# Performance work log

Hardware: AMD Instinct MI355X
Metric: run time of the kernel (lower is better)

Reference implementation:

```python
import jax, jax.numpy as jnp
import numpy as np

B, T, C, H = 2, 2048, 1024, 16
HD = C // H  # 64
EPS = 1e-5


def _ln(x, g, b):
    mu = jnp.mean(x, axis=-1, keepdims=True)
    var = jnp.var(x, axis=-1, keepdims=True)
    return (x - mu) * jax.lax.rsqrt(var + EPS) * g + b


def setup_inputs() -> dict:
    key = jax.random.key(0)
    ks = jax.random.split(key, 8)
    s = lambda n: 1.0 / np.sqrt(n)
    return {
        "x": jax.random.normal(ks[0], (B, T, C), dtype=jnp.float32),
        "ln1_g": jnp.ones((C,), jnp.float32), "ln1_b": jnp.zeros((C,), jnp.float32),
        "ln2_g": jnp.ones((C,), jnp.float32), "ln2_b": jnp.zeros((C,), jnp.float32),
        "w_in": jax.random.normal(ks[1], (C, 3 * C), jnp.float32) * s(C),
        "b_in": jnp.zeros((3 * C,), jnp.float32),
        "w_out": jax.random.normal(ks[2], (C, C), jnp.float32) * s(C),
        "b_out": jnp.zeros((C,), jnp.float32),
        "w_fc": jax.random.normal(ks[3], (C, 4 * C), jnp.float32) * s(C),
        "b_fc": jnp.zeros((4 * C,), jnp.float32),
        "w_proj": jax.random.normal(ks[4], (4 * C, C), jnp.float32) * s(4 * C),
        "b_proj": jnp.zeros((C,), jnp.float32),
    }


def reference(x, ln1_g, ln1_b, ln2_g, ln2_b, w_in, b_in, w_out, b_out,
              w_fc, b_fc, w_proj, b_proj):
    # --- residual 1: x + attn(ln1(x)) ---
    h = _ln(x, ln1_g, ln1_b)
    qkv = h @ w_in + b_in                          # (B,T,3C)
    # reshape to (B,T,H,3*HD) then chunk per head (matches torch code exactly)
    qkv = qkv.reshape(B, T, H, 3 * HD).transpose(0, 2, 1, 3)  # (B,H,T,3*HD)
    q, k, v = jnp.split(qkv, 3, axis=-1)           # each (B,H,T,HD)
    att = jnp.einsum('bhqd,bhkd->bhqk', q, k) / np.sqrt(HD)
    causal = jnp.tril(jnp.ones((T, T), bool))
    att = jnp.where(causal, att, -jnp.inf)
    att = jax.nn.softmax(att, axis=-1)
    o = jnp.einsum('bhqk,bhkd->bhqd', att, v)      # (B,H,T,HD)
    o = o.transpose(0, 2, 1, 3).reshape(B, T, C)
    x1 = x + (o @ w_out + b_out)
    # --- ln2 applied to residual stream, then residual 2 on top of ln2 output ---
    y = _ln(x1, ln2_g, ln2_b)
    mlp = jax.nn.gelu(y @ w_fc + b_fc, approximate=False) @ w_proj + b_proj
    return y + mlp
```

## Files before the change

### kernel.cpp

```cpp
#include <hip/hip_runtime.h>
#include <hip/hip_bf16.h>
#include <math.h>

typedef __bf16 bf16;
typedef __bf16 bf16x8 __attribute__((ext_vector_type(8)));
typedef __bf16 bf16x4 __attribute__((ext_vector_type(4)));
typedef float floatx4 __attribute__((ext_vector_type(4)));

#define B_ 2
#define T_ 2048
#define C_ 1024
#define H_ 16
#define HD_ 64

__device__ __forceinline__ void gload_lds16(const bf16* g, bf16* l) {
    __builtin_amdgcn_global_load_lds(
        (const __attribute__((address_space(1))) unsigned int*)(g),
        (__attribute__((address_space(3))) unsigned int*)(l), 16, 0, 0);
}

__global__ void transpose_all(const float* __restrict__ w_in, const float* __restrict__ w_out,
                              const float* __restrict__ w_fc, const float* __restrict__ w_proj,
                              bf16* __restrict__ o_in, bf16* __restrict__ o_out,
                              bf16* __restrict__ o_fc, bf16* __restrict__ o_proj) {
    int t = blockIdx.x;
    const float* src; bf16* dst; int K, N, idx;
    if (t < 3072)      { src = w_in;   dst = o_in;   K = 1024; N = 3072; idx = t; }
    else if (t < 4096) { src = w_out;  dst = o_out;  K = 1024; N = 1024; idx = t - 3072; }
    else if (t < 8192) { src = w_fc;   dst = o_fc;   K = 1024; N = 4096; idx = t - 4096; }
    else               { src = w_proj; dst = o_proj; K = 4096; N = 1024; idx = t - 8192; }
    int ntx = N >> 5;
    int nt = (idx % ntx) * 32, kt = (idx / ntx) * 32;
    __shared__ float tile[32][33];
    int tx = threadIdx.x, ty = threadIdx.y;
    #pragma unroll
    for (int i = 0; i < 32; i += 8)
        tile[ty + i][tx] = src[(size_t)(kt + ty + i) * N + nt + tx];
    __syncthreads();
    #pragma unroll
    for (int i = 0; i < 32; i += 8)
        dst[(size_t)(nt + ty + i) * K + kt + tx] = (bf16)tile[tx][ty + i];
}

__global__ __launch_bounds__(256) void ln_kernel(const float* __restrict__ x,
                                                 const float* __restrict__ g,
                                                 const float* __restrict__ b,
                                                 bf16* __restrict__ out_b,
                                                 float* __restrict__ out_f) {
    int row = blockIdx.x;
    int tid = threadIdx.x;
    const float* xr = x + (size_t)row * C_;
    float4 v = ((const float4*)xr)[tid];
    float s  = v.x + v.y + v.z + v.w;
    float ss = v.x * v.x + v.y * v.y + v.z * v.z + v.w * v.w;
    #pragma unroll
    for (int off = 32; off; off >>= 1) {
        s  += __shfl_down(s, off);
        ss += __shfl_down(ss, off);
    }
    __shared__ float red[8];
    int wid = tid >> 6;
    if ((tid & 63) == 0) { red[wid] = s; red[wid + 4] = ss; }
    __syncthreads();
    s  = red[0] + red[1] + red[2] + red[3];
    ss = red[4] + red[5] + red[6] + red[7];
    float mean = s * (1.0f / C_);
    float var  = ss * (1.0f / C_) - mean * mean;
    float rstd = rsqrtf(var + 1e-5f);
    float4 gv = ((const float4*)g)[tid];
    float4 bv = ((const float4*)b)[tid];
    float o0 = (v.x - mean) * rstd * gv.x + bv.x;
    float o1 = (v.y - mean) * rstd * gv.y + bv.y;
    float o2 = (v.z - mean) * rstd * gv.z + bv.z;
    float o3 = (v.w - mean) * rstd * gv.w + bv.w;
    bf16x4 ob = { (bf16)o0, (bf16)o1, (bf16)o2, (bf16)o3 };
    ((bf16x4*)out_b)[(size_t)row * 256 + tid] = ob;
    if (out_f) {
        float4 of; of.x = o0; of.y = o1; of.z = o2; of.w = o3;
        ((float4*)out_f)[(size_t)row * 256 + tid] = of;
    }
}

__device__ __forceinline__ float gelu_exact(float v) {
    return 0.5f * v * (1.0f + erff(v * 0.70710678118654752f));
}

template<int TN, int MODE>
__global__ __launch_bounds__(256) void gemm128(const bf16* __restrict__ A,
                                               const bf16* __restrict__ Bt,
                                               const float* __restrict__ bias,
                                               const float* __restrict__ add,
                                               void* __restrict__ out,
                                               int M, int N, int K) {
    constexpr int BN = TN / 32;
    __shared__ __align__(16) bf16 As[128 * 64];
    __shared__ __align__(16) bf16 Bs[TN * 64];

    int m0 = blockIdx.y * 128, n0 = blockIdx.x * TN;
    int tid = threadIdx.x;
    int wid = __builtin_amdgcn_readfirstlane(tid >> 6);
    int lane = tid & 63;
    int lm = lane & 15, quad = lane >> 4;
    int wm = (wid & 1) * 64;
    int wn = (wid >> 1) * (TN / 2);
    int lrow = lane >> 3;
    int lcol = (lane & 7) * 8;

    const bf16* Ablk = A  + (size_t)m0 * K;
    const bf16* Bblk = Bt + (size_t)n0 * K;

    floatx4 acc[4][BN];
    #pragma unroll
    for (int i = 0; i < 4; i++)
        #pragma unroll
        for (int j = 0; j < BN; j++) { floatx4 z = {0.f, 0.f, 0.f, 0.f}; acc[i][j] = z; }

    for (int k0 = 0; k0 < K; k0 += 64) {
        __syncthreads();
        #pragma unroll
        for (int c = 0; c < 4; c++) {
            int row = wid * 32 + c * 8;
            gload_lds16(Ablk + (size_t)(row + lrow) * K + k0 + lcol, As + row * 64);
        }
        #pragma unroll
        for (int c = 0; c < TN / 32; c++) {
            int row = wid * (TN / 4) + c * 8;
            gload_lds16(Bblk + (size_t)(row + lrow) * K + k0 + lcol, Bs + row * 64);
        }
        __syncthreads();
        #pragma unroll
        for (int kc = 0; kc < 2; kc++) {
            bf16x8 af[4], bfr[BN];
            #pragma unroll
            for (int i = 0; i < 4; i++)
                af[i] = *(const bf16x8*)(As + (wm + i * 16 + lm) * 64 + kc * 32 + quad * 8);
            #pragma unroll
            for (int j = 0; j < BN; j++)
                bfr[j] = *(const bf16x8*)(Bs + (wn + j * 16 + lm) * 64 + kc * 32 + quad * 8);
            #pragma unroll
            for (int i = 0; i < 4; i++)
                #pragma unroll
                for (int j = 0; j < BN; j++)
                    acc[i][j] = __builtin_amdgcn_mfma_f32_16x16x32_bf16(af[i], bfr[j], acc[i][j], 0, 0, 0);
        }
    }

    #pragma unroll
    for (int i = 0; i < 4; i++)
        #pragma unroll
        for (int j = 0; j < BN; j++) {
            int mbase = m0 + wm + i * 16 + quad * 4;
            int n     = n0 + wn + j * 16 + lm;
            float bsn = bias[n];
            #pragma unroll
            for (int r = 0; r < 4; r++) {
                size_t idx = (size_t)(mbase + r) * N + n;
                float v = acc[i][j][r] + bsn;
                if (MODE == 1) v = gelu_exact(v);
                if (MODE == 2) { ((float*)out)[idx] = v + add[idx]; }
                else           { ((bf16*)out)[idx] = (bf16)v; }
            }
        }
}

template<int MODE>
__global__ __launch_bounds__(256) void gemm_nrw(const bf16* __restrict__ A,
                                                const bf16* __restrict__ Bt,
                                                const float* __restrict__ bias,
                                                const float* __restrict__ add,
                                                void* __restrict__ out,
                                                int M, int N, int K) {
    __shared__ __align__(16) bf16 As[2][128 * 64];
    __shared__ __align__(16) bf16 Bs[2][64 * 64];

    int lin = blockIdx.x;
    int xcd = lin & 7, loc = lin >> 3;
    int m0 = (((xcd << 2) | (loc & 3))) * 128;
    int n0 = (loc >> 2) * 64;
    int tid = threadIdx.x;
    int wid = __builtin_amdgcn_readfirstlane(tid >> 6);
    int lane = tid & 63;
    int lm = lane & 15, quad = lane >> 4;
    int wm = (wid & 1) * 64;
    int wn = (wid >> 1) * 32;
    int lrow = lane >> 3;
    int lcol = (lane & 7) * 8;

    const bf16* Ablk = A  + (size_t)m0 * K;
    const bf16* Bblk = Bt + (size_t)n0 * K;

    floatx4 acc[4][2];
    #pragma unroll
    for (int i = 0; i < 4; i++)
        #pragma unroll
        for (int j = 0; j < 2; j++) { floatx4 z = {0.f, 0.f, 0.f, 0.f}; acc[i][j] = z; }

    #pragma unroll
    for (int c = 0; c < 4; c++) {
        int row = wid * 32 + c * 8;
        gload_lds16(Ablk + (size_t)(row + lrow) * K + lcol, &As[0][row * 64]);
    }
    #pragma unroll
    for (int c = 0; c < 2; c++) {
        int row = wid * 16 + c * 8;
        gload_lds16(Bblk + (size_t)(row + lrow) * K + lcol, &Bs[0][row * 64]);
    }

    int cur = 0;
    for (int k0 = 0; k0 < K; k0 += 64, cur ^= 1) {
        int nxt = cur ^ 1;
        if (k0 + 64 < K) {
            __builtin_amdgcn_s_barrier();
            __asm__ volatile("" ::: "memory");
            #pragma unroll
            for (int c = 0; c < 4; c++) {
                int row = wid * 32 + c * 8;
                gload_lds16(Ablk + (size_t)(row + lrow) * K + (k0 + 64) + lcol, &As[nxt][row * 64]);
            }
            #pragma unroll
            for (int c = 0; c < 2; c++) {
                int row = wid * 16 + c * 8;
                gload_lds16(Bblk + (size_t)(row + lrow) * K + (k0 + 64) + lcol, &Bs[nxt][row * 64]);
            }
            __asm__ volatile("s_waitcnt vmcnt(6)" ::: "memory");
        } else {
            __asm__ volatile("s_waitcnt vmcnt(0)" ::: "memory");
        }
        __builtin_amdgcn_s_barrier();
        __asm__ volatile("" ::: "memory");
        #pragma unroll
        for (int kc = 0; kc < 2; kc++) {
            bf16x8 af[4], bfr[2];
            #pragma unroll
            for (int i = 0; i < 4; i++)
                af[i] = *(const bf16x8*)(&As[cur][(wm + i * 16 + lm) * 64 + kc * 32 + quad * 8]);
            #pragma unroll
            for (int j = 0; j < 2; j++)
                bfr[j] = *(const bf16x8*)(&Bs[cur][(wn + j * 16 + lm) * 64 + kc * 32 + quad * 8]);
            #pragma unroll
            for (int i = 0; i < 4; i++)
                #pragma unroll
                for (int j = 0; j < 2; j++)
                    acc[i][j] = __builtin_amdgcn_mfma_f32_16x16x32_bf16(af[i], bfr[j], acc[i][j], 0, 0, 0);
        }
    }

    #pragma unroll
    for (int i = 0; i < 4; i++)
        #pragma unroll
        for (int j = 0; j < 2; j++) {
            int mbase = m0 + wm + i * 16 + quad * 4;
            int n     = n0 + wn + j * 16 + lm;
            float bsn = bias[n];
            #pragma unroll
            for (int r = 0; r < 4; r++) {
                size_t idx = (size_t)(mbase + r) * N + n;
                float v = acc[i][j][r] + bsn;
                if (MODE == 1) v = gelu_exact(v);
                if (MODE == 2) { ((float*)out)[idx] = v + add[idx]; }
                else           { ((bf16*)out)[idx] = (bf16)v; }
            }
        }
}

#define QT_ 128
#define KT_ 64

__global__ __launch_bounds__(256) void attn_mfma_kernel(const bf16* __restrict__ qkv,
                                                        bf16* __restrict__ o) {
    int bh = blockIdx.x;
    int b = bh >> 4, h = bh & 15;
    int q0 = (gridDim.y - 1 - blockIdx.y) * QT_;
    int tid = threadIdx.x, wid = tid >> 6, lane = tid & 63;
    int wm = wid * 32;
    int lm = lane & 15, quad = lane >> 4;
    int sw = lm & 7;

    const bf16* base = qkv + (size_t)b * T_ * (3 * C_) + h * (3 * HD_);

    __shared__ __align__(16) bf16 Ks[KT_][72];
    __shared__ __align__(16) bf16 Vt[HD_][72];
    __shared__ __align__(16) bf16 PsT[4][32][64];

    bf16x8 qf[2][2];
    #pragma unroll
    for (int am = 0; am < 2; am++)
        #pragma unroll
        for (int kc = 0; kc < 2; kc++) {
            int r = q0 + wm + am * 16 + lm;
            qf[am][kc] = *(const bf16x8*)(base + (size_t)r * (3 * C_) + kc * 32 + quad * 8);
        }

    floatx4 acc_o[2][4];
    #pragma unroll
    for (int am = 0; am < 2; am++)
        #pragma unroll
        for (int dn = 0; dn < 4; dn++) { floatx4 z = {0.f, 0.f, 0.f, 0.f}; acc_o[am][dn] = z; }
    float mst[2] = { -1e30f, -1e30f };
    float lst[2] = { 0.0f, 0.0f };

    int scol = (tid & 7) * 8;

    int kmax = q0 + QT_;
    for (int k0 = 0; k0 < kmax; k0 += KT_) {
        int kr0 = tid >> 3;
        bf16x8 kv0 = *(const bf16x8*)(base + (size_t)(k0 + kr0)      * (3 * C_) + HD_ + scol);
        bf16x8 kv1 = *(const bf16x8*)(base + (size_t)(k0 + kr0 + 32) * (3 * C_) + HD_ + scol);
        bf16x8 vv0 = *(const bf16x8*)(base + (size_t)(k0 + kr0)      * (3 * C_) + 2 * HD_ + scol);
        bf16x8 vv1 = *(const bf16x8*)(base + (size_t)(k0 + kr0 + 32) * (3 * C_) + 2 * HD_ + scol);
        __syncthreads();
        *(bf16x8*)(&Ks[kr0][scol])      = kv0;
        *(bf16x8*)(&Ks[kr0 + 32][scol]) = kv1;
        {
            int c = scol >> 3;
            int pk0 = (((kr0)       >> 3) ^ c) * 8 + (kr0 & 7);
            int pk1 = (((kr0 + 32)  >> 3) ^ c) * 8 + (kr0 & 7);
            #pragma unroll
            for (int j = 0; j < 8; j++) {
                Vt[scol + j][pk0] = vv0[j];
                Vt[scol + j][pk1] = vv1[j];
            }
        }
        __syncthreads();

        if (k0 <= q0 + wm + 31) {
            floatx4 st[4][2];
            #pragma unroll
            for (int bn = 0; bn < 4; bn++)
                #pragma unroll
                for (int am = 0; am < 2; am++) { floatx4 z = {0.f, 0.f, 0.f, 0.f}; st[bn][am] = z; }
            #pragma unroll
            for (int kc = 0; kc < 2; kc++) {
                bf16x8 kf[4];
                #pragma unroll
                for (int bn = 0; bn < 4; bn++)
                    kf[bn] = *(const bf16x8*)(&Ks[bn * 16 + lm][kc * 32 + quad * 8]);
                #pragma unroll
                for (int bn = 0; bn < 4; bn++)
                    #pragma unroll
                    for (int am = 0; am < 2; am++)
                        st[bn][am] = __builtin_amdgcn_mfma_f32_16x16x32_bf16(kf[bn], qf[am][kc], st[bn][am], 0, 0, 0);
            }

            float alpha_s[2];
            #pragma unroll
            for (int am = 0; am < 2; am++) {
                int gq = q0 + wm + am * 16 + lm;
                int need_mask = (k0 + KT_ - 1) > (q0 + wm + am * 16);
                float vv[4][4];
                float rm = -1e30f;
                #pragma unroll
                for (int bn = 0; bn < 4; bn++)
                    #pragma unroll
                    for (int r = 0; r < 4; r++) {
                        float sv = st[bn][am][r] * 0.125f;
                        int key = k0 + bn * 16 + quad * 4 + r;
                        sv = (!need_mask || key <= gq) ? sv : -1e30f;
                        vv[bn][r] = sv;
                        rm = fmaxf(rm, sv);
                    }
                rm = fmaxf(rm, __shfl_xor(rm, 16));
                rm = fmaxf(rm, __shfl_xor(rm, 32));
                float mold = mst[am];
                float mnew = fmaxf(mold, rm);
                float alpha = __expf(mold - mnew);
                mst[am] = mnew;
                float ps = 0.f;
                #pragma unroll
                for (int bn = 0; bn < 4; bn++) {
                    float p0 = __expf(vv[bn][0] - mnew);
                    float p1 = __expf(vv[bn][1] - mnew);
                    float p2 = __expf(vv[bn][2] - mnew);
                    float p3 = __expf(vv[bn][3] - mnew);
                    ps += (p0 + p1) + (p2 + p3);
                    bf16x4 pk = { (bf16)p0, (bf16)p1, (bf16)p2, (bf16)p3 };
                    int kb = bn * 2 + (quad >> 1);
                    int col = ((kb ^ sw) << 3) + (quad & 1) * 4;
                    *(bf16x4*)(&PsT[wid][am * 16 + lm][col]) = pk;
                }
                ps += __shfl_xor(ps, 16);
                ps += __shfl_xor(ps, 32);
                lst[am] = lst[am] * alpha + ps;
                alpha_s[am] = alpha;
            }

            #pragma unroll
            for (int am = 0; am < 2; am++)
                #pragma unroll
                for (int r = 0; r < 4; r++) {
                    float ar = __shfl(alpha_s[am], quad * 4 + r);
                    #pragma unroll
                    for (int dn = 0; dn < 4; dn++) acc_o[am][dn][r] *= ar;
                }

            __asm__ volatile("s_waitcnt lgkmcnt(0)" ::: "memory");

            #pragma unroll
            for (int kc = 0; kc < 2; kc++) {
                bf16x8 pa[2], vfr[4];
                #pragma unroll
                for (int am = 0; am < 2; am++)
                    pa[am] = *(const bf16x8*)(&PsT[wid][am * 16 + lm][((kc * 4 + quad) ^ sw) << 3]);
                #pragma unroll
                for (int dn = 0; dn < 4; dn++) {
                    int d = dn * 16 + lm;
                    int swd = (d >> 3) & 7;
                    vfr[dn] = *(const bf16x8*)(&Vt[d][(((kc * 4 + quad) ^ swd) << 3)]);
                }
                #pragma unroll
                for (int am = 0; am < 2; am++)
                    #pragma unroll
                    for (int dn = 0; dn < 4; dn++)
                        acc_o[am][dn] = __builtin_amdgcn_mfma_f32_16x16x32_bf16(pa[am], vfr[dn], acc_o[am][dn], 0, 0, 0);
            }
        }
    }

    #pragma unroll
    for (int am = 0; am < 2; am++) {
        float il = 1.0f / lst[am];
        #pragma unroll
        for (int r = 0; r < 4; r++) {
            float ir = __shfl(il, quad * 4 + r);
            int qrow = q0 + wm + am * 16 + quad * 4 + r;
            bf16* orow = o + ((size_t)b * T_ + qrow) * C_ + h * HD_;
            #pragma unroll
            for (int dn = 0; dn < 4; dn++)
                orow[dn * 16 + lm] = (bf16)(acc_o[am][dn][r] * ir);
        }
    }
}

extern "C" void kernel_launch(void* const* d_in, const int* in_sizes, int n_in,
                              void* d_out, int out_size, void* d_ws, size_t ws_size,
                              hipStream_t stream) {
    (void)in_sizes; (void)n_in; (void)out_size; (void)ws_size;
    const float* x      = (const float*)d_in[0];
    const float* ln1_g  = (const float*)d_in[1];
    const float* ln1_b  = (const float*)d_in[2];
    const float* ln2_g  = (const float*)d_in[3];
    const float* ln2_b  = (const float*)d_in[4];
    const float* w_in   = (const float*)d_in[5];
    const float* b_in   = (const float*)d_in[6];
    const float* w_out  = (const float*)d_in[7];
    const float* b_out  = (const float*)d_in[8];
    const float* w_fc   = (const float*)d_in[9];
    const float* b_fc   = (const float*)d_in[10];
    const float* w_proj = (const float*)d_in[11];
    const float* b_proj = (const float*)d_in[12];

    char* ws = (char*)d_ws;
    const size_t MB = 1024 * 1024;
    bf16*  w_inT   = (bf16*)(ws + 0);
    bf16*  w_outT  = (bf16*)(ws + 6 * MB);
    bf16*  w_fcT   = (bf16*)(ws + 8 * MB);
    bf16*  w_projT = (bf16*)(ws + 16 * MB);
    bf16*  qkv     = (bf16*)(ws + 24 * MB);
    bf16*  fc_act  = (bf16*)(ws + 24 * MB);
    bf16*  o_buf   = (bf16*)(ws + 56 * MB);
    bf16*  y_b     = (bf16*)(ws + 56 * MB);
    bf16*  h_b     = (bf16*)(ws + 64 * MB);
    float* x1      = (float*)(ws + 64 * MB);
    float* y_f     = (float*)(ws + 80 * MB);

    const int M = B_ * T_;

    transpose_all<<<12288, dim3(32, 8), 0, stream>>>(w_in, w_out, w_fc, w_proj,
                                                     w_inT, w_outT, w_fcT, w_projT);

    ln_kernel<<<M, 256, 0, stream>>>(x, ln1_g, ln1_b, h_b, nullptr);
    gemm128<128, 0><<<dim3(3 * C_ / 128, M / 128), 256, 0, stream>>>(h_b, w_inT, b_in, nullptr,
                                                                     qkv, M, 3 * C_, C_);
    attn_mfma_kernel<<<dim3(B_ * H_, T_ / QT_), 256, 0, stream>>>(qkv, o_buf);
    gemm_nrw<2><<<dim3((C_ / 64) * (M / 128)), 256, 0, stream>>>(o_buf, w_outT, b_out, x,
                                                                 x1, M, C_, C_);
    ln_kernel<<<M, 256, 0, stream>>>(x1, ln2_g, ln2_b, y_b, y_f);
    gemm128<128, 1><<<dim3(4 * C_ / 128, M / 128), 256, 0, stream>>>(y_b, w_fcT, b_fc, nullptr,
                                                                     fc_act, M, 4 * C_, C_);
    gemm_nrw<2><<<dim3((C_ / 64) * (M / 128)), 256, 0, stream>>>(fc_act, w_projT, b_proj, y_f,
                                                                 (float*)d_out, M, C_, 4 * C_);
}
```

Measured before the change: 391.1 us.

## Store activations and weights in MFMA fragment layout for LDS-free out/proj GEMMs

```diff
diff --git a/kernel.cpp b/kernel.cpp
--- a/kernel.cpp
+++ b/kernel.cpp
@@ -13,33 +13,57 @@
 #define H_ 16
 #define HD_ 64
 
+
 __device__ __forceinline__ void gload_lds16(const bf16* g, bf16* l) {
     __builtin_amdgcn_global_load_lds(
         (const __attribute__((address_space(1))) unsigned int*)(g),
         (__attribute__((address_space(3))) unsigned int*)(l), 16, 0, 0);
 }
 
-__global__ void transpose_all(const float* __restrict__ w_in, const float* __restrict__ w_out,
-                              const float* __restrict__ w_fc, const float* __restrict__ w_proj,
-                              bf16* __restrict__ o_in, bf16* __restrict__ o_out,
-                              bf16* __restrict__ o_fc, bf16* __restrict__ o_proj) {
+__global__ __launch_bounds__(256) void transpose_all(
+        const float* __restrict__ w_in, const float* __restrict__ w_out,
+        const float* __restrict__ w_fc, const float* __restrict__ w_proj,
+        bf16* __restrict__ o_in, bf16* __restrict__ o_out,
+        bf16* __restrict__ o_fc, bf16* __restrict__ o_proj) {
+    __shared__ float shf[64 * 33];
     int t = blockIdx.x;
-    const float* src; bf16* dst; int K, N, idx;
-    if (t < 3072)      { src = w_in;   dst = o_in;   K = 1024; N = 3072; idx = t; }
-    else if (t < 4096) { src = w_out;  dst = o_out;  K = 1024; N = 1024; idx = t - 3072; }
-    else if (t < 8192) { src = w_fc;   dst = o_fc;   K = 1024; N = 4096; idx = t - 4096; }
-    else               { src = w_proj; dst = o_proj; K = 4096; N = 1024; idx = t - 8192; }
-    int ntx = N >> 5;
-    int nt = (idx % ntx) * 32, kt = (idx / ntx) * 32;
-    __shared__ float tile[32][33];
-    int tx = threadIdx.x, ty = threadIdx.y;
-    #pragma unroll
-    for (int i = 0; i < 32; i += 8)
-        tile[ty + i][tx] = src[(size_t)(kt + ty + i) * N + nt + tx];
-    __syncthreads();
-    #pragma unroll
-    for (int i = 0; i < 32; i += 8)
-        dst[(size_t)(nt + ty + i) * K + kt + tx] = (bf16)tile[tx][ty + i];
+    int tid = threadIdx.x;
+    if (t < 7168) {
+        const float* src; bf16* dst; int K, N, idx;
+        if (t < 3072) { src = w_in; dst = o_in; K = 1024; N = 3072; idx = t; }
+        else          { src = w_fc; dst = o_fc; K = 1024; N = 4096; idx = t - 3072; }
+        int ntx = N >> 5;
+        int nt = (idx % ntx) * 32, kt = (idx / ntx) * 32;
+        int tx = tid & 31, ty = tid >> 5;
+        #pragma unroll
+        for (int i = 0; i < 32; i += 8)
+            shf[(ty + i) * 33 + tx] = src[(size_t)(kt + ty + i) * N + nt + tx];
+        __syncthreads();
+        #pragma unroll
+        for (int i = 0; i < 32; i += 8)
+            dst[(size_t)(nt + ty + i) * K + kt + tx] = (bf16)shf[tx * 33 + ty + i];
+    } else {
+        const float* src; bf16* dst; int K, idx;
+        if (t < 7680) { src = w_out;  dst = o_out;  K = 1024; idx = t - 7168; }
+        else          { src = w_proj; dst = o_proj; K = 4096; idx = t - 7680; }
+        const int N = 1024;
+        int n0 = (idx & 31) * 32, k0 = (idx >> 5) * 64;
+        int col = tid & 31, kr = tid >> 5;
+        #pragma unroll
+        for (int s = 0; s < 8; s++)
+            shf[(kr + s * 8) * 33 + col] = src[(size_t)(k0 + kr + s * 8) * N + n0 + col];
+        __syncthreads();
+        int tl = tid >> 6, l = tid & 63;
+        int ntl = tl & 1, kcl = tl >> 1;
+        int rr = ntl * 16 + (l & 15);
+        int qd = l >> 4;
+        bf16x8 v;
+        #pragma unroll
+        for (int e = 0; e < 8; e++)
+            v[e] = (bf16)shf[(kcl * 32 + qd * 8 + e) * 33 + rr];
+        size_t nt_g = (n0 >> 4) + ntl, kc_g = (k0 >> 5) + kcl;
+        *(bf16x8*)(dst + (nt_g * (K >> 5) + kc_g) * 512 + l * 8) = v;
+    }
 }
 
 __global__ __launch_bounds__(256) void ln_kernel(const float* __restrict__ x,
@@ -85,35 +109,34 @@
     return 0.5f * v * (1.0f + erff(v * 0.70710678118654752f));
 }
 
-template<int TN, int MODE>
+template<int MODE>
 __global__ __launch_bounds__(256) void gemm128(const bf16* __restrict__ A,
                                                const bf16* __restrict__ Bt,
                                                const float* __restrict__ bias,
-                                               const float* __restrict__ add,
                                                void* __restrict__ out,
                                                int M, int N, int K) {
-    constexpr int BN = TN / 32;
-    __shared__ __align__(16) bf16 As[128 * 64];
-    __shared__ __align__(16) bf16 Bs[TN * 64];
-
-    int m0 = blockIdx.y * 128, n0 = blockIdx.x * TN;
+    __shared__ __align__(16) bf16 smem[128 * 136];
+    bf16* As = smem;
+    bf16* Bs = smem + 128 * 64;
+
+    int m0 = blockIdx.y * 128, n0 = blockIdx.x * 128;
     int tid = threadIdx.x;
     int wid = __builtin_amdgcn_readfirstlane(tid >> 6);
     int lane = tid & 63;
     int lm = lane & 15, quad = lane >> 4;
     int wm = (wid & 1) * 64;
-    int wn = (wid >> 1) * (TN / 2);
+    int wn = (wid >> 1) * 64;
     int lrow = lane >> 3;
     int lcol = (lane & 7) * 8;
 
     const bf16* Ablk = A  + (size_t)m0 * K;
     const bf16* Bblk = Bt + (size_t)n0 * K;
 
-    floatx4 acc[4][BN];
+    floatx4 acc[4][4];
     #pragma unroll
     for (int i = 0; i < 4; i++)
         #pragma unroll
-        for (int j = 0; j < BN; j++) { floatx4 z = {0.f, 0.f, 0.f, 0.f}; acc[i][j] = z; }
+        for (int j = 0; j < 4; j++) { floatx4 z = {0.f, 0.f, 0.f, 0.f}; acc[i][j] = z; }
 
     for (int k0 = 0; k0 < K; k0 += 64) {
         __syncthreads();
@@ -123,71 +146,84 @@
             gload_lds16(Ablk + (size_t)(row + lrow) * K + k0 + lcol, As + row * 64);
         }
         #pragma unroll
-        for (int c = 0; c < TN / 32; c++) {
-            int row = wid * (TN / 4) + c * 8;
+        for (int c = 0; c < 4; c++) {
+            int row = wid * 32 + c * 8;
             gload_lds16(Bblk + (size_t)(row + lrow) * K + k0 + lcol, Bs + row * 64);
         }
         __syncthreads();
         #pragma unroll
         for (int kc = 0; kc < 2; kc++) {
-            bf16x8 af[4], bfr[BN];
+            bf16x8 af[4], bfr[4];
             #pragma unroll
             for (int i = 0; i < 4; i++)
                 af[i] = *(const bf16x8*)(As + (wm + i * 16 + lm) * 64 + kc * 32 + quad * 8);
             #pragma unroll
-            for (int j = 0; j < BN; j++)
+            for (int j = 0; j < 4; j++)
                 bfr[j] = *(const bf16x8*)(Bs + (wn + j * 16 + lm) * 64 + kc * 32 + quad * 8);
             #pragma unroll
             for (int i = 0; i < 4; i++)
                 #pragma unroll
-                for (int j = 0; j < BN; j++)
+                for (int j = 0; j < 4; j++)
                     acc[i][j] = __builtin_amdgcn_mfma_f32_16x16x32_bf16(af[i], bfr[j], acc[i][j], 0, 0, 0);
         }
     }
 
-    #pragma unroll
-    for (int i = 0; i < 4; i++)
-        #pragma unroll
-        for (int j = 0; j < BN; j++) {
-            int mbase = m0 + wm + i * 16 + quad * 4;
-            int n     = n0 + wn + j * 16 + lm;
-            float bsn = bias[n];
-            #pragma unroll
-            for (int r = 0; r < 4; r++) {
-                size_t idx = (size_t)(mbase + r) * N + n;
-                float v = acc[i][j][r] + bsn;
-                if (MODE == 1) v = gelu_exact(v);
-                if (MODE == 2) { ((float*)out)[idx] = v + add[idx]; }
-                else           { ((bf16*)out)[idx] = (bf16)v; }
-            }
-        }
-}
-
-template<int MODE>
-__global__ __launch_bounds__(256) void gemm_nrw(const bf16* __restrict__ A,
-                                                const bf16* __restrict__ Bt,
-                                                const float* __restrict__ bias,
-                                                const float* __restrict__ add,
-                                                void* __restrict__ out,
-                                                int M, int N, int K) {
-    __shared__ __align__(16) bf16 As[2][128 * 64];
-    __shared__ __align__(16) bf16 Bs[2][64 * 64];
-
+    if (MODE == 0) {
+        #pragma unroll
+        for (int i = 0; i < 4; i++)
+            #pragma unroll
+            for (int j = 0; j < 4; j++) {
+                int mbase = m0 + wm + i * 16 + quad * 4;
+                int n     = n0 + wn + j * 16 + lm;
+                float bsn = bias[n];
+                #pragma unroll
+                for (int r = 0; r < 4; r++)
+                    ((bf16*)out)[(size_t)(mbase + r) * N + n] = (bf16)(acc[i][j][r] + bsn);
+            }
+    } else {
+        __syncthreads();
+        #pragma unroll
+        for (int i = 0; i < 4; i++)
+            #pragma unroll
+            for (int j = 0; j < 4; j++) {
+                int n = n0 + wn + j * 16 + lm;
+                float bsn = bias[n];
+                #pragma unroll
+                for (int r = 0; r < 4; r++)
+                    smem[(wm + i * 16 + quad * 4 + r) * 136 + wn + j * 16 + lm] =
+                        (bf16)gelu_exact(acc[i][j][r] + bsn);
+            }
+        __syncthreads();
+        bf16* ob = (bf16*)out;
+        int kcb = n0 >> 5;
+        #pragma unroll
+        for (int p = 0; p < 8; p++) {
+            int tl = wid * 8 + p;
+            int mtl = tl >> 2, kcl = tl & 3;
+            bf16x8 v = *(const bf16x8*)&smem[(mtl * 16 + lm) * 136 + kcl * 32 + quad * 8];
+            *(bf16x8*)(ob + (((size_t)((m0 >> 4) + mtl) * (N >> 5) + kcb + kcl) * 512) + lane * 8) = v;
+        }
+    }
+}
+
+__global__ __launch_bounds__(256) void gemm_direct(const bf16* __restrict__ Af,
+                                                   const bf16* __restrict__ Bf,
+                                                   const float* __restrict__ bias,
+                                                   const float* __restrict__ add,
+                                                   float* __restrict__ out,
+                                                   int M, int N, int K) {
     int lin = blockIdx.x;
     int xcd = lin & 7, loc = lin >> 3;
-    int m0 = (((xcd << 2) | (loc & 3))) * 128;
+    int m0 = ((xcd << 2) | (loc & 3)) * 128;
     int n0 = (loc >> 2) * 64;
     int tid = threadIdx.x;
     int wid = __builtin_amdgcn_readfirstlane(tid >> 6);
     int lane = tid & 63;
     int lm = lane & 15, quad = lane >> 4;
-    int wm = (wid & 1) * 64;
-    int wn = (wid >> 1) * 32;
-    int lrow = lane >> 3;
-    int lcol = (lane & 7) * 8;
-
-    const bf16* Ablk = A  + (size_t)m0 * K;
-    const bf16* Bblk = Bt + (size_t)n0 * K;
+    int wm = (wid & 1) * 64, wn = (wid >> 1) * 32;
+    int KC = K >> 5;
+    const bf16* Ab = Af + ((size_t)((m0 + wm) >> 4) * KC) * 512 + lane * 8;
+    const bf16* Bb = Bf + ((size_t)((n0 + wn) >> 4) * KC) * 512 + lane * 8;
 
     floatx4 acc[4][2];
     #pragma unroll
@@ -195,53 +231,48 @@
         #pragma unroll
         for (int j = 0; j < 2; j++) { floatx4 z = {0.f, 0.f, 0.f, 0.f}; acc[i][j] = z; }
 
-    #pragma unroll
-    for (int c = 0; c < 4; c++) {
-        int row = wid * 32 + c * 8;
-        gload_lds16(Ablk + (size_t)(row + lrow) * K + lcol, &As[0][row * 64]);
-    }
-    #pragma unroll
-    for (int c = 0; c < 2; c++) {
-        int row = wid * 16 + c * 8;
-        gload_lds16(Bblk + (size_t)(row + lrow) * K + lcol, &Bs[0][row * 64]);
-    }
-
-    int cur = 0;
-    for (int k0 = 0; k0 < K; k0 += 64, cur ^= 1) {
-        int nxt = cur ^ 1;
-        if (k0 + 64 < K) {
-            __builtin_amdgcn_s_barrier();
-            __asm__ volatile("" ::: "memory");
-            #pragma unroll
-            for (int c = 0; c < 4; c++) {
-                int row = wid * 32 + c * 8;
-                gload_lds16(Ablk + (size_t)(row + lrow) * K + (k0 + 64) + lcol, &As[nxt][row * 64]);
-            }
-            #pragma unroll
-            for (int c = 0; c < 2; c++) {
-                int row = wid * 16 + c * 8;
-                gload_lds16(Bblk + (size_t)(row + lrow) * K + (k0 + 64) + lcol, &Bs[nxt][row * 64]);
-            }
-            __asm__ volatile("s_waitcnt vmcnt(6)" ::: "memory");
-        } else {
-            __asm__ volatile("s_waitcnt vmcnt(0)" ::: "memory");
-        }
-        __builtin_amdgcn_s_barrier();
-        __asm__ volatile("" ::: "memory");
-        #pragma unroll
-        for (int kc = 0; kc < 2; kc++) {
-            bf16x8 af[4], bfr[2];
+    bf16x8 ac[4][2], bc[2][2], an[4][2], bn[2][2];
+    #pragma unroll
+    for (int i = 0; i < 4; i++)
+        #pragma unroll
+        for (int c = 0; c < 2; c++)
+            ac[i][c] = *(const bf16x8*)(Ab + ((size_t)i * KC + c) * 512);
+    #pragma unroll
+    for (int j = 0; j < 2; j++)
+        #pragma unroll
+        for (int c = 0; c < 2; c++)
+            bc[j][c] = *(const bf16x8*)(Bb + ((size_t)j * KC + c) * 512);
+
+    for (int kc0 = 0; kc0 < KC; kc0 += 2) {
+        bool pre = (kc0 + 2) < KC;
+        if (pre) {
             #pragma unroll
             for (int i = 0; i < 4; i++)
-                af[i] = *(const bf16x8*)(&As[cur][(wm + i * 16 + lm) * 64 + kc * 32 + quad * 8]);
+                #pragma unroll
+                for (int c = 0; c < 2; c++)
+                    an[i][c] = *(const bf16x8*)(Ab + ((size_t)i * KC + kc0 + 2 + c) * 512);
             #pragma unroll
             for (int j = 0; j < 2; j++)
-                bfr[j] = *(const bf16x8*)(&Bs[cur][(wn + j * 16 + lm) * 64 + kc * 32 + quad * 8]);
+                #pragma unroll
+                for (int c = 0; c < 2; c++)
+                    bn[j][c] = *(const bf16x8*)(Bb + ((size_t)j * KC + kc0 + 2 + c) * 512);
+        }
+        #pragma unroll
+        for (int c = 0; c < 2; c++)
             #pragma unroll
             for (int i = 0; i < 4; i++)
                 #pragma unroll
                 for (int j = 0; j < 2; j++)
-                    acc[i][j] = __builtin_amdgcn_mfma_f32_16x16x32_bf16(af[i], bfr[j], acc[i][j], 0, 0, 0);
+                    acc[i][j] = __builtin_amdgcn_mfma_f32_16x16x32_bf16(ac[i][c], bc[j][c], acc[i][j], 0, 0, 0);
+        if (pre) {
+            #pragma unroll
+            for (int i = 0; i < 4; i++)
+                #pragma unroll
+                for (int c = 0; c < 2; c++) ac[i][c] = an[i][c];
+            #pragma unroll
+            for (int j = 0; j < 2; j++)
+                #pragma unroll
+                for (int c = 0; c < 2; c++) bc[j][c] = bn[j][c];
         }
     }
 
@@ -255,10 +286,7 @@
             #pragma unroll
             for (int r = 0; r < 4; r++) {
                 size_t idx = (size_t)(mbase + r) * N + n;
-                float v = acc[i][j][r] + bsn;
-                if (MODE == 1) v = gelu_exact(v);
-                if (MODE == 2) { ((float*)out)[idx] = v + add[idx]; }
-                else           { ((bf16*)out)[idx] = (bf16)v; }
+                out[idx] = acc[i][j][r] + bsn + add[idx];
             }
         }
 }
@@ -267,7 +295,7 @@
 #define KT_ 64
 
 __global__ __launch_bounds__(256) void attn_mfma_kernel(const bf16* __restrict__ qkv,
-                                                        bf16* __restrict__ o) {
+                                                        bf16* __restrict__ of) {
     int bh = blockIdx.x;
     int b = bh >> 4, h = bh & 15;
     int q0 = (gridDim.y - 1 - blockIdx.y) * QT_;
@@ -422,13 +450,20 @@
         #pragma unroll
         for (int r = 0; r < 4; r++) {
             float ir = __shfl(il, quad * 4 + r);
-            int qrow = q0 + wm + am * 16 + quad * 4 + r;
-            bf16* orow = o + ((size_t)b * T_ + qrow) * C_ + h * HD_;
             #pragma unroll
             for (int dn = 0; dn < 4; dn++)
-                orow[dn * 16 + lm] = (bf16)(acc_o[am][dn][r] * ir);
-        }
-    }
+                PsT[wid][am * 16 + quad * 4 + r][dn * 16 + lm] = (bf16)(acc_o[am][dn][r] * ir);
+        }
+    }
+    __asm__ volatile("s_waitcnt lgkmcnt(0)" ::: "memory");
+    size_t mtb = ((size_t)b * T_ + q0 + wm) >> 4;
+    #pragma unroll
+    for (int am = 0; am < 2; am++)
+        #pragma unroll
+        for (int kcl = 0; kcl < 2; kcl++) {
+            bf16x8 v = *(const bf16x8*)&PsT[wid][am * 16 + lm][kcl * 32 + quad * 8];
+            *(bf16x8*)(of + ((mtb + am) * (C_ >> 5) + (h * 2 + kcl)) * 512 + lane * 8) = v;
+        }
 }
 
 extern "C" void kernel_launch(void* const* d_in, const int* in_sizes, int n_in,
@@ -452,12 +487,12 @@
     char* ws = (char*)d_ws;
     const size_t MB = 1024 * 1024;
     bf16*  w_inT   = (bf16*)(ws + 0);
-    bf16*  w_outT  = (bf16*)(ws + 6 * MB);
+    bf16*  w_outF  = (bf16*)(ws + 6 * MB);
     bf16*  w_fcT   = (bf16*)(ws + 8 * MB);
-    bf16*  w_projT = (bf16*)(ws + 16 * MB);
+    bf16*  w_projF = (bf16*)(ws + 16 * MB);
     bf16*  qkv     = (bf16*)(ws + 24 * MB);
-    bf16*  fc_act  = (bf16*)(ws + 24 * MB);
-    bf16*  o_buf   = (bf16*)(ws + 56 * MB);
+    bf16*  fc_frag = (bf16*)(ws + 24 * MB);
+    bf16*  o_frag  = (bf16*)(ws + 56 * MB);
     bf16*  y_b     = (bf16*)(ws + 56 * MB);
     bf16*  h_b     = (bf16*)(ws + 64 * MB);
     float* x1      = (float*)(ws + 64 * MB);
@@ -465,18 +500,17 @@
 
     const int M = B_ * T_;
 
-    transpose_all<<<12288, dim3(32, 8), 0, stream>>>(w_in, w_out, w_fc, w_proj,
-                                                     w_inT, w_outT, w_fcT, w_projT);
+    transpose_all<<<9728, 256, 0, stream>>>(w_in, w_out, w_fc, w_proj,
+                                            w_inT, w_outF, w_fcT, w_projF);
 
     ln_kernel<<<M, 256, 0, stream>>>(x, ln1_g, ln1_b, h_b, nullptr);
-    gemm128<128, 0><<<dim3(3 * C_ / 128, M / 128), 256, 0, stream>>>(h_b, w_inT, b_in, nullptr,
-                                                                     qkv, M, 3 * C_, C_);
-    attn_mfma_kernel<<<dim3(B_ * H_, T_ / QT_), 256, 0, stream>>>(qkv, o_buf);
-    gemm_nrw<2><<<dim3((C_ / 64) * (M / 128)), 256, 0, stream>>>(o_buf, w_outT, b_out, x,
-                                                                 x1, M, C_, C_);
+    gemm128<0><<<dim3(3 * C_ / 128, M / 128), 256, 0, stream>>>(h_b, w_inT, b_in,
+                                                                qkv, M, 3 * C_, C_);
+    attn_mfma_kernel<<<dim3(B_ * H_, T_ / QT_), 256, 0, stream>>>(qkv, o_frag);
+    gemm_direct<<<512, 256, 0, stream>>>(o_frag, w_outF, b_out, x, x1, M, C_, C_);
     ln_kernel<<<M, 256, 0, stream>>>(x1, ln2_g, ln2_b, y_b, y_f);
-    gemm128<128, 1><<<dim3(4 * C_ / 128, M / 128), 256, 0, stream>>>(y_b, w_fcT, b_fc, nullptr,
-                                                                     fc_act, M, 4 * C_, C_);
-    gemm_nrw<2><<<dim3((C_ / 64) * (M / 128)), 256, 0, stream>>>(fc_act, w_projT, b_proj, y_f,
-                                                                 (float*)d_out, M, C_, 4 * C_);
-}
+    gemm128<1><<<dim3(4 * C_ / 128, M / 128), 256, 0, stream>>>(y_b, w_fcT, b_fc,
+                                                                fc_frag, M, 4 * C_, C_);
+    gemm_direct<<<512, 256, 0, stream>>>(fc_frag, w_projF, b_proj, y_f,
+                                         (float*)d_out, M, C_, 4 * C_);
+}
```

Result: faster. 373.9 us (-4.4%).
